# Performance work log

Hardware: AMD Instinct MI355X
Metric: run time of the kernel (lower is better)

The kernel has to match this reference:

```python
import jax, jax.numpy as jnp
import numpy as np

P = 16          # patch size (square)
HEADS = 8
DH = 64         # dim per head
SCALE = DH ** -0.5
EPS = 1e-5


def layernorm(x, g, b):
    mu = x.mean(-1, keepdims=True)
    var = ((x - mu) ** 2).mean(-1, keepdims=True)
    return (x - mu) * jax.lax.rsqrt(var + EPS) * g + b


def sattn(q, k, v):
    # q:[..., i, d], k/v:[..., j, d]; q already scaled
    sim = jnp.einsum('...id,...jd->...ij', q, k)
    a = jax.nn.softmax(sim, axis=-1)
    return jnp.einsum('...ij,...jd->...id', a, v)


def split_heads(t, b, N):
    return t.reshape(b, N, HEADS, DH).transpose(0, 2, 1, 3).reshape(b * HEADS, N, DH)


def merge_heads(t, b, N):
    return t.reshape(b, HEADS, N, DH).transpose(0, 2, 1, 3).reshape(b, N, HEADS * DH)


def qkv_cls(x, ln_g, ln_b, qkv_w):
    b, N, _ = x.shape
    xn = layernorm(x, ln_g, ln_b)
    q, k, v = jnp.split(xn @ qkv_w, 3, axis=-1)
    q = split_heads(q, b, N) * SCALE
    k = split_heads(k, b, N)
    v = split_heads(v, b, N)
    cls_out = sattn(q[:, :1], k, v)          # cls attends to everything
    return q[:, 1:], k[:, 1:], v[:, 1:], k[:, :1], v[:, :1], cls_out


def time_attention(x, ln_g, ln_b, qkv_w, out_w, out_b, f, n):
    b, N, _ = x.shape
    q_, k_, v_, cls_k, cls_v, cls_out = qkv_cls(x, ln_g, ln_b, qkv_w)
    bh = b * HEADS
    resh = lambda t: t.reshape(bh, f, n, DH).transpose(0, 2, 1, 3)  # 'b (f n) d -> (b n) f d' kept as [bh,n,f,d]
    q_, k_, v_ = resh(q_), resh(k_), resh(v_)
    ck = jnp.broadcast_to(cls_k[:, None], (bh, n, 1, DH))
    cv = jnp.broadcast_to(cls_v[:, None], (bh, n, 1, DH))
    out = sattn(q_, jnp.concatenate([ck, k_], 2), jnp.concatenate([cv, v_], 2))
    out = out.transpose(0, 2, 1, 3).reshape(bh, f * n, DH)
    out = jnp.concatenate([cls_out, out], axis=1)
    return merge_heads(out, b, N) @ out_w + out_b


def space_attention(x, ln_g, ln_b, qkv_w, out_w, out_b, f, n):
    b, N, _ = x.shape
    q_, k_, v_, cls_k, cls_v, cls_out = qkv_cls(x, ln_g, ln_b, qkv_w)
    bh = b * HEADS
    resh = lambda t: t.reshape(bh, f, n, DH)  # 'b (f n) d -> (b f) n d' kept as [bh,f,n,d]
    q_, k_, v_ = resh(q_), resh(k_), resh(v_)
    m = n // 2
    ck = jnp.broadcast_to(cls_k[:, None], (bh, f, 1, DH))
    cv = jnp.broadcast_to(cls_v[:, None], (bh, f, 1, DH))
    # mutual attention: first half queries attend to [cls, second half], and vice versa
    out1 = sattn(q_[:, :, :m], jnp.concatenate([ck, k_[:, :, m:]], 2), jnp.concatenate([cv, v_[:, :, m:]], 2))
    out2 = sattn(q_[:, :, m:], jnp.concatenate([ck, k_[:, :, :m]], 2), jnp.concatenate([cv, v_[:, :, :m]], 2))
    out = jnp.concatenate([out1, out2], axis=2).reshape(bh, f * n, DH)
    out = jnp.concatenate([cls_out, out], axis=1)
    return merge_heads(out, b, N) @ out_w + out_b


def geglu_ff(x, ln_g, ln_b, w1, b1, w2, b2):
    xn = layernorm(x, ln_g, ln_b)
    h = xn @ w1 + b1
    u, g = jnp.split(h, 2, axis=-1)
    return (u * jax.nn.gelu(g, approximate=False)) @ w2 + b2


def setup_inputs() -> dict:
    key = jax.random.key(0)
    ks = jax.random.split(key, 12)
    D, DEPTH, NC = 512, 12, 60
    inner = HEADS * DH
    B, F, C, H, W = 1, 4, 3, 480, 640
    n = (H // P) * (W // P)        # 1200
    N = F * n + 1                  # 4801
    pd = C * P * P                 # 768
    s = 0.02
    rn = lambda k, sh: jax.random.normal(k, sh, jnp.float32) * s
    z = lambda sh: jnp.zeros(sh, jnp.float32)
    o = lambda sh: jnp.ones(sh, jnp.float32)
    return {
        'video': jax.random.normal(ks[0], (B, F, C, H, W), jnp.float32),
        'patch_w': rn(ks[1], (pd, D)), 'patch_b': z((D,)),
        'pos_emb': rn(ks[2], (N, D)),
        'cls_token': rn(ks[3], (1, D)),
        't_ln_g': o((DEPTH, D)), 't_ln_b': z((DEPTH, D)),
        't_qkv_w': rn(ks[4], (DEPTH, D, 3 * inner)),
        't_out_w': rn(ks[5], (DEPTH, inner, D)), 't_out_b': z((DEPTH, D)),
        's_ln_g': o((DEPTH, D)), 's_ln_b': z((DEPTH, D)),
        's_qkv_w': rn(ks[6], (DEPTH, D, 3 * inner)),
        's_out_w': rn(ks[7], (DEPTH, inner, D)), 's_out_b': z((DEPTH, D)),
        'f_ln_g': o((DEPTH, D)), 'f_ln_b': z((DEPTH, D)),
        'f_w1': rn(ks[8], (DEPTH, D, 8 * D)), 'f_b1': z((DEPTH, 8 * D)),
        'f_w2': rn(ks[9], (DEPTH, 4 * D, D)), 'f_b2': z((DEPTH, D)),
        'o_ln_g': o((D,)), 'o_ln_b': z((D,)),
        'o_w': rn(ks[10], (D, NC)), 'o_b': z((NC,)),
    }


def reference(video, patch_w, patch_b, pos_emb, cls_token,
              t_ln_g, t_ln_b, t_qkv_w, t_out_w, t_out_b,
              s_ln_g, s_ln_b, s_qkv_w, s_out_w, s_out_b,
              f_ln_g, f_ln_b, f_w1, f_b1, f_w2, f_b2,
              o_ln_g, o_ln_b, o_w, o_b):
    b, f, c, H, W = video.shape
    hh, ww = H // P, W // P
    n = hh * ww
    wh = ww // 2
    half = W // 2

    def patchify(v):  # v: [b,f,c,H,W/2] -> [b, f*hh*wh, P*P*c]
        v = v.reshape(b, f, c, hh, P, wh, P)
        v = v.transpose(0, 1, 3, 5, 4, 6, 2)  # b f h w p1 p2 c
        return v.reshape(b, f * hh * wh, P * P * c)

    tok = jnp.concatenate([patchify(video[..., :half]), patchify(video[..., half:])], axis=1)
    tok = tok @ patch_w + patch_b
    x = jnp.concatenate([jnp.broadcast_to(cls_token[None], (b, 1, tok.shape[-1])), tok], axis=1)
    x = x + pos_emb[: x.shape[1]]

    depth = t_qkv_w.shape[0]
    for i in range(depth):
        x = time_attention(x, t_ln_g[i], t_ln_b[i], t_qkv_w[i], t_out_w[i], t_out_b[i], f, n) + x
        x = space_attention(x, s_ln_g[i], s_ln_b[i], s_qkv_w[i], s_out_w[i], s_out_b[i], f, n) + x
        x = geglu_ff(x, f_ln_g[i], f_ln_b[i], f_w1[i], f_b1[i], f_w2[i], f_b2[i]) + x

    cls = layernorm(x[:, 0], o_ln_g, o_ln_b)
    return cls @ o_w + o_b
```

## Files before the change

### kernel.cpp

```cpp
#include <hip/hip_runtime.h>
#include <cmath>


#define NT      4801
#define NP      4800
#define MP      4864
#define DM      512
#define QKV_ST  1536
#define LN_EPS  1e-5f
#define NCH     49

typedef __attribute__((ext_vector_type(8))) short bf16x8;
typedef __attribute__((ext_vector_type(4))) float f32x4;

__device__ __forceinline__ unsigned short f2b(float f) {
    union { float f; unsigned int u; } x; x.f = f;
    unsigned int r = (x.u + 0x7FFFu + ((x.u >> 16) & 1u)) >> 16;
    return (unsigned short)r;
}
__device__ __forceinline__ float b2f(unsigned short b) {
    union { unsigned int u; float f; } x; x.u = ((unsigned int)b) << 16;
    return x.f;
}
__device__ __forceinline__ unsigned int pack2(float a, float b) {
    return (unsigned int)f2b(a) | ((unsigned int)f2b(b) << 16);
}

__device__ __forceinline__ void gl_lds16(const void* g, void* l) {
    __builtin_amdgcn_global_load_lds(
        (__attribute__((address_space(1))) unsigned int*)(unsigned long long)(uintptr_t)g,
        (__attribute__((address_space(3))) unsigned int*)l, 16, 0, 0);
}

__device__ __forceinline__ void xcd_remap(int& bx, int& by, int& bz) {
    const int gx = gridDim.x, gy = gridDim.y;
    const int nwg = gx * gy * gridDim.z;
    const int orig = (blockIdx.z * gy + blockIdx.y) * gx + blockIdx.x;
    const int q = nwg >> 3, r = nwg & 7;
    const int xcd = orig & 7, idx = orig >> 3;
    const int id = (xcd < r ? xcd * (q + 1) : r * (q + 1) + (xcd - r) * q) + idx;
    bx = id % gx;
    const int t = id / gx;
    by = t % gy;
    bz = t / gy;
}

__global__ void patchify_kernel(const float* __restrict__ video, unsigned short* __restrict__ out)
{
    int idx = blockIdx.x * 256 + threadIdx.x;
    if (idx >= NP * 768) return;
    int tok = idx / 768, e = idx % 768;
    int c  = e % 3;
    int pe = e / 3;
    int p2 = pe % 16, p1 = pe / 16;
    int half = tok / 2400, r = tok % 2400;
    int f = r / 600, rr = r % 600;
    int hi = rr / 20, wi = rr % 20;
    int row = hi * 16 + p1;
    int col = half * 320 + wi * 16 + p2;
    out[idx] = f2b(video[(((size_t)f * 3 + c) * 480 + row) * 640 + col]);
}

__global__ void cls_init_kernel(const float* __restrict__ cls_token,
                                const float* __restrict__ pos, float* __restrict__ X)
{
    int d = blockIdx.x * 256 + threadIdx.x;
    if (d < DM) X[d] = cls_token[d] + pos[d];
}

__global__ void posx_init(const float* __restrict__ pos, float* __restrict__ X)
{
    int i = blockIdx.x * 256 + threadIdx.x;
    if (i < NP * DM / 4)
        ((float4*)(X + DM))[i] = ((const float4*)(pos + DM))[i];
}

__device__ __forceinline__ void transpose_tile(const float* __restrict__ in,
                                               unsigned short* __restrict__ out,
                                               int K, int N, int tile)
{
    __shared__ float T[32][33];
    int ntk = K / 32;
    int kt = tile % ntk, nt = tile / ntk;
    int k0 = kt * 32, n0 = nt * 32;
    int tx = threadIdx.x & 31, ty = threadIdx.x >> 5;
    #pragma unroll
    for (int i = 0; i < 4; i++)
        T[ty + 8 * i][tx] = in[(size_t)(k0 + ty + 8 * i) * N + n0 + tx];
    __syncthreads();
    #pragma unroll
    for (int i = 0; i < 4; i++)
        out[(size_t)(n0 + ty + 8 * i) * K + k0 + tx] = f2b(T[tx][ty + 8 * i]);
}

__global__ __launch_bounds__(256) void convertT_layer(
    const float* __restrict__ w0, const float* __restrict__ w1,
    const float* __restrict__ w2, const float* __restrict__ w3,
    const float* __restrict__ w4, const float* __restrict__ w5,
    unsigned short* __restrict__ out)
{
    int t = blockIdx.x;
    if      (t <  768) transpose_tile(w0, out + 0,       512, 1536, t);
    else if (t < 1024) transpose_tile(w1, out + 786432,  512,  512, t - 768);
    else if (t < 1792) transpose_tile(w2, out + 1048576, 512, 1536, t - 1024);
    else if (t < 2048) transpose_tile(w3, out + 1835008, 512,  512, t - 1792);
    else if (t < 4096) transpose_tile(w4, out + 2097152, 512, 4096, t - 2048);
    else               transpose_tile(w5, out + 4194304, 2048, 512, t - 4096);
}

__global__ __launch_bounds__(256) void convertT_one(
    const float* __restrict__ in, unsigned short* __restrict__ out, int K, int N)
{
    transpose_tile(in, out, K, N, blockIdx.x);
}

template<bool OB16>
__global__ __launch_bounds__(256, 2) void mfma_gemm(
    const unsigned short* __restrict__ A, const unsigned short* __restrict__ BT,
    const float* __restrict__ bias, const float* __restrict__ add,
    void* __restrict__ C, int Mv, int N, int K)
{
    __shared__ short Asm[2][128 * 64];
    __shared__ short Bsm[2][128 * 64];
    int bx, by, bz; xcd_remap(bx, by, bz); (void)bz;
    const int tid = threadIdx.x, w = tid >> 6, lane = tid & 63;
    const int row0 = by * 128, col0 = bx * 128;
    const int wm = w >> 1, wn = w & 1;
    const int l15 = lane & 15, quad = lane >> 4;

    f32x4 acc[4][4] = {};

    int ar[4], aq[4];
    #pragma unroll
    for (int i = 0; i < 4; i++) {
        int c = (w * 4 + i) * 64 + lane;
        ar[i] = c >> 3;
        aq[i] = (c & 7) ^ ((c >> 3) & 7);
    }
    const unsigned short* Ab = A  + (size_t)row0 * K;
    const unsigned short* Bb = BT + (size_t)col0 * K;

    #pragma unroll
    for (int i = 0; i < 4; i++) {
        gl_lds16(Ab + (size_t)ar[i] * K + aq[i] * 8, &Asm[0][(w * 4 + i) * 512]);
        gl_lds16(Bb + (size_t)ar[i] * K + aq[i] * 8, &Bsm[0][(w * 4 + i) * 512]);
    }

    const int nt = K >> 6;
    int cur = 0;
    for (int t = 0; t < nt; t++) {
        if (t + 1 < nt) {
            const int k0 = (t + 1) << 6;
            #pragma unroll
            for (int i = 0; i < 4; i++) {
                gl_lds16(Ab + (size_t)ar[i] * K + k0 + aq[i] * 8,
                         &Asm[cur ^ 1][(w * 4 + i) * 512]);
                gl_lds16(Bb + (size_t)ar[i] * K + k0 + aq[i] * 8,
                         &Bsm[cur ^ 1][(w * 4 + i) * 512]);
            }
            asm volatile("s_waitcnt vmcnt(8)\ns_barrier" ::: "memory");
        } else {
            asm volatile("s_waitcnt vmcnt(0)\ns_barrier" ::: "memory");
        }
        const short* As = Asm[cur];
        const short* Bs = Bsm[cur];
        #pragma unroll
        for (int ks = 0; ks < 2; ks++) {
            bf16x8 af[4], bfr[4];
            #pragma unroll
            for (int i = 0; i < 4; i++) {
                int m  = wm * 64 + i * 16 + l15;
                af[i]  = *(const bf16x8*)&As[m * 64 + (((ks * 4 + quad) ^ (m & 7))) * 8];
                int n  = wn * 64 + i * 16 + l15;
                bfr[i] = *(const bf16x8*)&Bs[n * 64 + (((ks * 4 + quad) ^ (n & 7))) * 8];
            }
            #pragma unroll
            for (int i = 0; i < 4; i++)
                #pragma unroll
                for (int j = 0; j < 4; j++)
                    acc[i][j] = __builtin_amdgcn_mfma_f32_16x16x32_bf16(
                                    af[i], bfr[j], acc[i][j], 0, 0, 0);
        }
        asm volatile("s_barrier" ::: "memory");
        cur ^= 1;
    }

    #pragma unroll
    for (int i = 0; i < 4; i++) {
        #pragma unroll
        for (int r = 0; r < 4; r++) {
            int row = row0 + wm * 64 + i * 16 + quad * 4 + r;
            if (row >= Mv) continue;
            #pragma unroll
            for (int j = 0; j < 4; j++) {
                int col = col0 + wn * 64 + j * 16 + l15;
                float v = acc[i][j][r];
                if (bias) v += bias[col];
                if (add)  v += add[(size_t)row * N + col];
                if (OB16) ((unsigned short*)C)[(size_t)row * N + col] = f2b(v);
                else      ((float*)C)[(size_t)row * N + col] = v;
            }
        }
    }
}

template<int SPLITS>
__global__ __launch_bounds__(256, 2) void mfma_gemm_sk(
    const unsigned short* __restrict__ A, const unsigned short* __restrict__ BT,
    const float* __restrict__ bias, float* __restrict__ C, int Mv, int N, int K)
{
    __shared__ short Asm[2][128 * 64];
    __shared__ short Bsm[2][128 * 64];
    int bx, by, bz; xcd_remap(bx, by, bz);
    const int tid = threadIdx.x, w = tid >> 6, lane = tid & 63;
    const int row0 = by * 128, col0 = bx * 128;
    const int wm = w >> 1, wn = w & 1;
    const int l15 = lane & 15, quad = lane >> 4;
    const int kchunk = K / SPLITS;
    const int kbeg = bz * kchunk;

    f32x4 acc[4][4] = {};

    int ar[4], aq[4];
    #pragma unroll
    for (int i = 0; i < 4; i++) {
        int c = (w * 4 + i) * 64 + lane;
        ar[i] = c >> 3;
        aq[i] = (c & 7) ^ ((c >> 3) & 7);
    }
    const unsigned short* Ab = A  + (size_t)row0 * K + kbeg;
    const unsigned short* Bb = BT + (size_t)col0 * K + kbeg;

    #pragma unroll
    for (int i = 0; i < 4; i++) {
        gl_lds16(Ab + (size_t)ar[i] * K + aq[i] * 8, &Asm[0][(w * 4 + i) * 512]);
        gl_lds16(Bb + (size_t)ar[i] * K + aq[i] * 8, &Bsm[0][(w * 4 + i) * 512]);
    }

    const int nt = kchunk >> 6;
    int cur = 0;
    for (int t = 0; t < nt; t++) {
        if (t + 1 < nt) {
            const int k0 = (t + 1) << 6;
            #pragma unroll
            for (int i = 0; i < 4; i++) {
                gl_lds16(Ab + (size_t)ar[i] * K + k0 + aq[i] * 8,
                         &Asm[cur ^ 1][(w * 4 + i) * 512]);
                gl_lds16(Bb + (size_t)ar[i] * K + k0 + aq[i] * 8,
                         &Bsm[cur ^ 1][(w * 4 + i) * 512]);
            }
            asm volatile("s_waitcnt vmcnt(8)\ns_barrier" ::: "memory");
        } else {
            asm volatile("s_waitcnt vmcnt(0)\ns_barrier" ::: "memory");
        }
        const short* As = Asm[cur];
        const short* Bs = Bsm[cur];
        #pragma unroll
        for (int ks = 0; ks < 2; ks++) {
            bf16x8 af[4], bfr[4];
            #pragma unroll
            for (int i = 0; i < 4; i++) {
                int m  = wm * 64 + i * 16 + l15;
                af[i]  = *(const bf16x8*)&As[m * 64 + (((ks * 4 + quad) ^ (m & 7))) * 8];
                int n  = wn * 64 + i * 16 + l15;
                bfr[i] = *(const bf16x8*)&Bs[n * 64 + (((ks * 4 + quad) ^ (n & 7))) * 8];
            }
            #pragma unroll
            for (int i = 0; i < 4; i++)
                #pragma unroll
                for (int j = 0; j < 4; j++)
                    acc[i][j] = __builtin_amdgcn_mfma_f32_16x16x32_bf16(
                                    af[i], bfr[j], acc[i][j], 0, 0, 0);
        }
        asm volatile("s_barrier" ::: "memory");
        cur ^= 1;
    }

    const bool addb = (bz == 0) && (bias != nullptr);
    #pragma unroll
    for (int i = 0; i < 4; i++) {
        #pragma unroll
        for (int r = 0; r < 4; r++) {
            int row = row0 + wm * 64 + i * 16 + quad * 4 + r;
            if (row >= Mv) continue;
            #pragma unroll
            for (int j = 0; j < 4; j++) {
                int col = col0 + wn * 64 + j * 16 + l15;
                float v = acc[i][j][r];
                if (addb) v += bias[col];
                unsafeAtomicAdd(&C[(size_t)row * N + col], v);
            }
        }
    }
}

__global__ __launch_bounds__(256, 2) void mfma_ff1_geglu(
    const unsigned short* __restrict__ A, const unsigned short* __restrict__ BT,
    const float* __restrict__ b1, unsigned short* __restrict__ out, int Mv)
{
    __shared__ short Asm[128 * 64];
    __shared__ short Bu[128 * 64];
    __shared__ short Bg[128 * 64];
    int bx, by, bz; xcd_remap(bx, by, bz); (void)bz;
    const int tid = threadIdx.x, w = tid >> 6, lane = tid & 63;
    const int row0 = by * 128, colu0 = bx * 128;
    const int wm = w >> 1, wn = w & 1;
    const int l15 = lane & 15, quad = lane >> 4;

    f32x4 au[4][4] = {};
    f32x4 ag[4][4] = {};

    int ar[4], aq[4];
    #pragma unroll
    for (int i = 0; i < 4; i++) {
        int c = (w * 4 + i) * 64 + lane;
        ar[i] = c >> 3;
        aq[i] = (c & 7) ^ ((c >> 3) & 7);
    }
    const unsigned short* Ab  = A  + (size_t)row0 * 512;
    const unsigned short* Bub = BT + (size_t)colu0 * 512;
    const unsigned short* Bgb = BT + (size_t)(colu0 + 2048) * 512;

    for (int k0 = 0; k0 < 512; k0 += 64) {
        #pragma unroll
        for (int i = 0; i < 4; i++) {
            gl_lds16(Ab  + (size_t)ar[i] * 512 + k0 + aq[i] * 8, &Asm[(w * 4 + i) * 512]);
            gl_lds16(Bub + (size_t)ar[i] * 512 + k0 + aq[i] * 8, &Bu[(w * 4 + i) * 512]);
            gl_lds16(Bgb + (size_t)ar[i] * 512 + k0 + aq[i] * 8, &Bg[(w * 4 + i) * 512]);
        }
        __syncthreads();
        #pragma unroll
        for (int ks = 0; ks < 2; ks++) {
            bf16x8 af[4], bu[4], bg[4];
            #pragma unroll
            for (int i = 0; i < 4; i++) {
                int m = wm * 64 + i * 16 + l15;
                int p = (((ks * 4 + quad) ^ (m & 7))) * 8;
                af[i] = *(const bf16x8*)&Asm[m * 64 + p];
                int n = wn * 64 + i * 16 + l15;
                int pb = (((ks * 4 + quad) ^ (n & 7))) * 8;
                bu[i] = *(const bf16x8*)&Bu[n * 64 + pb];
                bg[i] = *(const bf16x8*)&Bg[n * 64 + pb];
            }
            #pragma unroll
            for (int i = 0; i < 4; i++)
                #pragma unroll
                for (int j = 0; j < 4; j++) {
                    au[i][j] = __builtin_amdgcn_mfma_f32_16x16x32_bf16(
                                   af[i], bu[j], au[i][j], 0, 0, 0);
                    ag[i][j] = __builtin_amdgcn_mfma_f32_16x16x32_bf16(
                                   af[i], bg[j], ag[i][j], 0, 0, 0);
                }
        }
        __syncthreads();
    }

    #pragma unroll
    for (int i = 0; i < 4; i++) {
        #pragma unroll
        for (int r = 0; r < 4; r++) {
            int row = row0 + wm * 64 + i * 16 + quad * 4 + r;
            if (row >= Mv) continue;
            #pragma unroll
            for (int j = 0; j < 4; j++) {
                int col = colu0 + wn * 64 + j * 16 + l15;
                float u = au[i][j][r] + b1[col];
                float g = ag[i][j][r] + b1[col + 2048];
                float h = u * 0.5f * g * (1.f + erff(g * 0.70710678f));
                out[(size_t)row * 2048 + col] = f2b(h);
            }
        }
    }
}

__global__ __launch_bounds__(256) void ln_bf16(
    const float* __restrict__ x, const float* __restrict__ g,
    const float* __restrict__ b, unsigned short* __restrict__ y, int M)
{
    int wid = threadIdx.x >> 6, lane = threadIdx.x & 63;
    int row = blockIdx.x * 4 + wid;
    if (row >= M) return;
    const float4* xr = (const float4*)(x + (size_t)row * DM);
    float4 v0 = xr[lane * 2], v1 = xr[lane * 2 + 1];
    float s  = v0.x + v0.y + v0.z + v0.w + v1.x + v1.y + v1.z + v1.w;
    float s2 = v0.x*v0.x + v0.y*v0.y + v0.z*v0.z + v0.w*v0.w
             + v1.x*v1.x + v1.y*v1.y + v1.z*v1.z + v1.w*v1.w;
    #pragma unroll
    for (int off = 32; off >= 1; off >>= 1) {
        s  += __shfl_xor(s, off);
        s2 += __shfl_xor(s2, off);
    }
    float mu = s * (1.f / DM);
    float var = s2 * (1.f / DM) - mu * mu;
    float r = rsqrtf(var + LN_EPS);
    const float4* gv = (const float4*)g;
    const float4* bv = (const float4*)b;
    unsigned int* yr = (unsigned int*)(y + (size_t)row * DM);
    #pragma unroll
    for (int i = 0; i < 2; i++) {
        float4 v = (i == 0) ? v0 : v1;
        float4 gg = gv[lane * 2 + i], bb = bv[lane * 2 + i];
        float ox = (v.x - mu) * r * gg.x + bb.x;
        float oy = (v.y - mu) * r * gg.y + bb.y;
        float oz = (v.z - mu) * r * gg.z + bb.z;
        float ow = (v.w - mu) * r * gg.w + bb.w;
        yr[lane * 4 + i * 2 + 0] = pack2(ox, oy);
        yr[lane * 4 + i * 2 + 1] = pack2(oz, ow);
    }
}

__global__ __launch_bounds__(256, 4) void time_attn4(
    const unsigned short* __restrict__ qkv, unsigned short* __restrict__ out)
{
    int tid = threadIdx.x;
    int dq = tid & 3, tl = tid >> 2;
    int b = blockIdx.x;
    int h = b / 75;
    int j = (b - h * 75) * 64 + tl;
    int pos = j % 1200;
    int d0 = dq * 16;
    union { bf16x8 v; unsigned short u[8]; } ld;
    float q[16];
    const unsigned short* qp = qkv + (size_t)(j + 1) * QKV_ST + h * 64 + d0;
    #pragma unroll
    for (int c = 0; c < 2; c++) {
        ld.v = *(const bf16x8*)(qp + c * 8);
        #pragma unroll
        for (int e = 0; e < 8; e++) q[c * 8 + e] = b2f(ld.u[e]) * 0.125f;
    }
    int rows[5] = {0, pos + 1, pos + 1201, pos + 2401, pos + 3601};
    float s[5];
    #pragma unroll
    for (int kk = 0; kk < 5; kk++) {
        const unsigned short* kp = qkv + (size_t)rows[kk] * QKV_ST + 512 + h * 64 + d0;
        float ss = 0.f;
        #pragma unroll
        for (int c = 0; c < 2; c++) {
            ld.v = *(const bf16x8*)(kp + c * 8);
            #pragma unroll
            for (int e = 0; e < 8; e++) ss += q[c * 8 + e] * b2f(ld.u[e]);
        }
        ss += __shfl_xor(ss, 1);
        ss += __shfl_xor(ss, 2);
        s[kk] = ss;
    }
    float mx = s[0];
    #pragma unroll
    for (int kk = 1; kk < 5; kk++) mx = fmaxf(mx, s[kk]);
    float e5[5], l = 0.f;
    #pragma unroll
    for (int kk = 0; kk < 5; kk++) { e5[kk] = __expf(s[kk] - mx); l += e5[kk]; }
    float rl = 1.f / l;
    float acc[16];
    #pragma unroll
    for (int d = 0; d < 16; d++) acc[d] = 0.f;
    #pragma unroll
    for (int kk = 0; kk < 5; kk++) {
        float p = e5[kk] * rl;
        const unsigned short* vp = qkv + (size_t)rows[kk] * QKV_ST + 1024 + h * 64 + d0;
        #pragma unroll
        for (int c = 0; c < 2; c++) {
            ld.v = *(const bf16x8*)(vp + c * 8);
            #pragma unroll
            for (int e = 0; e < 8; e++) acc[c * 8 + e] += p * b2f(ld.u[e]);
        }
    }
    unsigned int* op = (unsigned int*)(out + (size_t)(j + 1) * DM + h * 64 + d0);
    #pragma unroll
    for (int d2 = 0; d2 < 8; d2++) op[d2] = pack2(acc[2 * d2], acc[2 * d2 + 1]);
}

#define SPAD 72
__global__ __launch_bounds__(256, 2) void space_attn_mfma(
    const unsigned short* __restrict__ qkv, unsigned short* __restrict__ out)
{
    __shared__ short Ksm[64 * SPAD];
    __shared__ short VTsm[64 * SPAD];
    __shared__ short Psm[4][32 * SPAD];
    int qt = blockIdx.x, h = blockIdx.y, g = blockIdx.z;
    int f = g >> 1, half = g & 1;
    int tid = threadIdx.x, w = tid >> 6, lane = tid & 63;
    int l15 = lane & 15, quad = lane >> 4;

    int qrow_base = qt * 128 + w * 32;
    int qb = 1 + f * 1200 + half * 600;
    int kb = 1 + f * 1200 + (1 - half) * 600;

    bf16x8 aQ[2][2];
    #pragma unroll
    for (int mf = 0; mf < 2; mf++) {
        int qr = qrow_base + mf * 16 + l15;
        int qtok = qb + ((qr < 600) ? qr : 0);
        const unsigned short* qp = qkv + (size_t)qtok * QKV_ST + h * 64;
        #pragma unroll
        for (int ks = 0; ks < 2; ks++)
            aQ[mf][ks] = *(const bf16x8*)(qp + ks * 32 + quad * 8);
    }

    f32x4 O[2][4] = {};
    float mrow[2][4], lrow[2][4];
    #pragma unroll
    for (int mf = 0; mf < 2; mf++)
        #pragma unroll
        for (int r = 0; r < 4; r++) { mrow[mf][r] = -1e30f; lrow[mf][r] = 0.f; }

    for (int kt = 0; kt < 10; kt++) {
        __syncthreads();
        #pragma unroll
        for (int it = 0; it < 2; it++) {
            int c = tid + it * 256;
            int row = c >> 3, dc = (c & 7) * 8;
            int kidx = kt * 64 + row;
            int tok = (kidx == 0) ? 0 : ((kidx <= 600) ? kb + kidx - 1 : 0);
            const unsigned short* kp = qkv + (size_t)tok * QKV_ST + 512 + h * 64 + dc;
            *(bf16x8*)&Ksm[row * SPAD + dc] = *(const bf16x8*)kp;
            union { bf16x8 v; unsigned short u[8]; } vv;
            vv.v = *(const bf16x8*)(kp + 512);
            #pragma unroll
            for (int e = 0; e < 8; e++)
                VTsm[(dc + e) * SPAD + row] = vv.u[e];
        }
        __syncthreads();

        f32x4 S[2][4] = {};
        #pragma unroll
        for (int ks = 0; ks < 2; ks++) {
            bf16x8 bK[4];
            #pragma unroll
            for (int nf = 0; nf < 4; nf++)
                bK[nf] = *(const bf16x8*)&Ksm[(nf * 16 + l15) * SPAD + ks * 32 + quad * 8];
            #pragma unroll
            for (int mf = 0; mf < 2; mf++)
                #pragma unroll
                for (int nf = 0; nf < 4; nf++)
                    S[mf][nf] = __builtin_amdgcn_mfma_f32_16x16x32_bf16(
                                    aQ[mf][ks], bK[nf], S[mf][nf], 0, 0, 0);
        }

        #pragma unroll
        for (int mf = 0; mf < 2; mf++) {
            float pv[4][4];
            float lm[4] = {-1e30f, -1e30f, -1e30f, -1e30f};
            #pragma unroll
            for (int nf = 0; nf < 4; nf++) {
                int kidx = kt * 64 + nf * 16 + l15;
                bool valid = kidx <= 600;
                #pragma unroll
                for (int r = 0; r < 4; r++) {
                    float s = valid ? S[mf][nf][r] * 0.125f : -1e30f;
                    pv[nf][r] = s;
                    lm[r] = fmaxf(lm[r], s);
                }
            }
            #pragma unroll
            for (int off = 1; off < 16; off <<= 1)
                #pragma unroll
                for (int r = 0; r < 4; r++)
                    lm[r] = fmaxf(lm[r], __shfl_xor(lm[r], off));
            #pragma unroll
            for (int r = 0; r < 4; r++) {
                float nm = fmaxf(mrow[mf][r], lm[r]);
                float c = __expf(mrow[mf][r] - nm);
                mrow[mf][r] = nm;
                lrow[mf][r] *= c;
                #pragma unroll
                for (int nf = 0; nf < 4; nf++) O[mf][nf][r] *= c;
            }
            float rs[4] = {0.f, 0.f, 0.f, 0.f};
            #pragma unroll
            for (int nf = 0; nf < 4; nf++)
                #pragma unroll
                for (int r = 0; r < 4; r++) {
                    float p = __expf(pv[nf][r] - mrow[mf][r]);
                    pv[nf][r] = p;
                    rs[r] += p;
                }
            #pragma unroll
            for (int off = 1; off < 16; off <<= 1)
                #pragma unroll
                for (int r = 0; r < 4; r++)
                    rs[r] += __shfl_xor(rs[r], off);
            #pragma unroll
            for (int r = 0; r < 4; r++) lrow[mf][r] += rs[r];
            #pragma unroll
            for (int nf = 0; nf < 4; nf++)
                #pragma unroll
                for (int r = 0; r < 4; r++)
                    Psm[w][(mf * 16 + quad * 4 + r) * SPAD + nf * 16 + l15] = (short)f2b(pv[nf][r]);
        }
        asm volatile("s_waitcnt lgkmcnt(0)" ::: "memory");

        #pragma unroll
        for (int ks2 = 0; ks2 < 2; ks2++) {
            bf16x8 aP[2], bV[4];
            #pragma unroll
            for (int mf = 0; mf < 2; mf++)
                aP[mf] = *(const bf16x8*)&Psm[w][(mf * 16 + l15) * SPAD + ks2 * 32 + quad * 8];
            #pragma unroll
            for (int nf = 0; nf < 4; nf++)
                bV[nf] = *(const bf16x8*)&VTsm[(nf * 16 + l15) * SPAD + ks2 * 32 + quad * 8];
            #pragma unroll
            for (int mf = 0; mf < 2; mf++)
                #pragma unroll
                for (int nf = 0; nf < 4; nf++)
                    O[mf][nf] = __builtin_amdgcn_mfma_f32_16x16x32_bf16(
                                    aP[mf], bV[nf], O[mf][nf], 0, 0, 0);
        }
    }

    #pragma unroll
    for (int mf = 0; mf < 2; mf++)
        #pragma unroll
        for (int r = 0; r < 4; r++) {
            int qr = qrow_base + mf * 16 + quad * 4 + r;
            if (qr >= 600) continue;
            int qtok = qb + qr;
            float rl = 1.f / lrow[mf][r];
            #pragma unroll
            for (int nf = 0; nf < 4; nf++)
                out[(size_t)qtok * DM + h * 64 + nf * 16 + l15] = f2b(O[mf][nf][r] * rl);
        }
}

__global__ __launch_bounds__(256) void cls_attn_part(
    const unsigned short* __restrict__ qkv, float* __restrict__ part)
{
    int ch = blockIdx.x, h = blockIdx.y;
    int wid = threadIdx.x >> 6, lane = threadIdx.x & 63;
    __shared__ float sm[4], sl[4], sa[4][64];
    float qv = b2f(qkv[h * 64 + lane]) * 0.125f;
    int k0 = ch * 100 + wid * 25;
    float m = -1e30f, l = 0.f, acc = 0.f;
    for (int i = 0; i < 25; i += 2) {
        int key0 = k0 + i, key1 = key0 + 1;
        bool ok0 = key0 < NT;
        bool ok1 = (i + 1 < 25) && (key1 < NT);
        const unsigned short* kr0 = qkv + (size_t)(ok0 ? key0 : 0) * QKV_ST + 512 + h * 64;
        const unsigned short* kr1 = qkv + (size_t)(ok1 ? key1 : 0) * QKV_ST + 512 + h * 64;
        float s0 = qv * b2f(kr0[lane]);
        float v0 = b2f(kr0[512 + lane]);
        float s1 = qv * b2f(kr1[lane]);
        float v1 = b2f(kr1[512 + lane]);
        #pragma unroll
        for (int off = 32; off >= 1; off >>= 1) {
            s0 += __shfl_xor(s0, off);
            s1 += __shfl_xor(s1, off);
        }
        float nm = m;
        if (ok0) nm = fmaxf(nm, s0);
        if (ok1) nm = fmaxf(nm, s1);
        float c  = __expf(m - nm);
        float p0 = ok0 ? __expf(s0 - nm) : 0.f;
        float p1 = ok1 ? __expf(s1 - nm) : 0.f;
        l   = l * c + p0 + p1;
        acc = acc * c + p0 * v0 + p1 * v1;
        m = nm;
    }
    if (lane == 0) { sm[wid] = m; sl[wid] = l; }
    sa[wid][lane] = acc;
    __syncthreads();
    if (wid == 0) {
        float M2 = fmaxf(fmaxf(sm[0], sm[1]), fmaxf(sm[2], sm[3]));
        float L = 0.f, o = 0.f;
        #pragma unroll
        for (int w = 0; w < 4; w++) {
            float c = __expf(sm[w] - M2);
            L += sl[w] * c;
            o += sa[w][lane] * c;
        }
        float* p = part + ((size_t)h * NCH + ch) * 68;
        if (lane == 0) { p[0] = M2; p[1] = L; }
        p[4 + lane] = o;
    }
}

__global__ __launch_bounds__(64) void cls_attn_reduce(
    const float* __restrict__ part, unsigned short* __restrict__ out)
{
    int h = blockIdx.x, lane = threadIdx.x;
    float m = -1e30f, l = 0.f, acc = 0.f;
    for (int c = 0; c < NCH; c++) {
        const float* p = part + ((size_t)h * NCH + c) * 68;
        float cm = p[0], cl = p[1], ca = p[4 + lane];
        float nm = fmaxf(m, cm);
        float e1 = __expf(m - nm), e2 = __expf(cm - nm);
        l   = l * e1 + cl * e2;
        acc = acc * e1 + ca * e2;
        m = nm;
    }
    out[h * 64 + lane] = f2b(acc / l);
}

__global__ __launch_bounds__(64) void head_kernel(
    const float* __restrict__ x, const float* __restrict__ g,
    const float* __restrict__ b, const float* __restrict__ w,
    const float* __restrict__ ob, float* __restrict__ out)
{
    __shared__ float xn[DM];
    int lane = threadIdx.x;
    const float4* xr = (const float4*)x;
    float4 v0 = xr[lane * 2], v1 = xr[lane * 2 + 1];
    float s  = v0.x + v0.y + v0.z + v0.w + v1.x + v1.y + v1.z + v1.w;
    float s2 = v0.x*v0.x + v0.y*v0.y + v0.z*v0.z + v0.w*v0.w
             + v1.x*v1.x + v1.y*v1.y + v1.z*v1.z + v1.w*v1.w;
    #pragma unroll
    for (int off = 32; off >= 1; off >>= 1) {
        s  += __shfl_xor(s, off);
        s2 += __shfl_xor(s2, off);
    }
    float mu = s * (1.f / DM);
    float var = s2 * (1.f / DM) - mu * mu;
    float r = rsqrtf(var + LN_EPS);
    #pragma unroll
    for (int i = 0; i < 8; i++) {
        int d = lane * 8 + i;
        xn[d] = (x[d] - mu) * r * g[d] + b[d];
    }
    __syncthreads();
    if (lane < 60) {
        float a = ob[lane];
        for (int d = 0; d < DM; d++) a += xn[d] * w[d * 60 + lane];
        out[lane] = a;
    }
}

extern "C" void kernel_launch(void* const* d_in, const int* in_sizes, int n_in,
                              void* d_out, int out_size, void* d_ws, size_t ws_size,
                              hipStream_t stream)
{
    const float* video     = (const float*)d_in[0];
    const float* patch_w   = (const float*)d_in[1];
    const float* patch_b   = (const float*)d_in[2];
    const float* pos_emb   = (const float*)d_in[3];
    const float* cls_token = (const float*)d_in[4];
    const float* t_ln_g    = (const float*)d_in[5];
    const float* t_ln_b    = (const float*)d_in[6];
    const float* t_qkv_w   = (const float*)d_in[7];
    const float* t_out_w   = (const float*)d_in[8];
    const float* t_out_b   = (const float*)d_in[9];
    const float* s_ln_g    = (const float*)d_in[10];
    const float* s_ln_b    = (const float*)d_in[11];
    const float* s_qkv_w   = (const float*)d_in[12];
    const float* s_out_w   = (const float*)d_in[13];
    const float* s_out_b   = (const float*)d_in[14];
    const float* f_ln_g    = (const float*)d_in[15];
    const float* f_ln_b    = (const float*)d_in[16];
    const float* f_w1      = (const float*)d_in[17];
    const float* f_b1      = (const float*)d_in[18];
    const float* f_w2      = (const float*)d_in[19];
    const float* f_b2      = (const float*)d_in[20];
    const float* o_ln_g    = (const float*)d_in[21];
    const float* o_ln_b    = (const float*)d_in[22];
    const float* o_w       = (const float*)d_in[23];
    const float* o_b       = (const float*)d_in[24];

    char* ws = (char*)d_ws;
    size_t o = 0;
    float*          X    = (float*)(ws + o);          o += (size_t)(MP + 1) * 512 * 4;
    unsigned short* XN   = (unsigned short*)(ws + o); o += (size_t)MP * 512 * 2;
    unsigned short* QKV  = (unsigned short*)(ws + o); o += (size_t)MP * 1536 * 2;
    unsigned short* H16  = (unsigned short*)(ws + o); o += (size_t)MP * 4096 * 2;
    unsigned short* MID  = (unsigned short*)(ws + o); o += (size_t)MP * 2048 * 2;
    unsigned short* PT   = (unsigned short*)(ws + o); o += (size_t)MP * 768 * 2;
    unsigned short* W16  = (unsigned short*)(ws + o); o += (size_t)5242880 * 2;
    unsigned short* PW16 = (unsigned short*)(ws + o); o += (size_t)512 * 768 * 2;
    float*          CP   = (float*)(ws + o);          o += (size_t)8 * NCH * 68 * 4;

    patchify_kernel<<<(NP * 768 + 255) / 256, 256, 0, stream>>>(video, PT);
    cls_init_kernel<<<2, 256, 0, stream>>>(cls_token, pos_emb, X);
    posx_init<<<NP * DM / 4 / 256, 256, 0, stream>>>(pos_emb, X);
    convertT_one<<<(768 / 32) * (512 / 32), 256, 0, stream>>>(patch_w, PW16, 768, 512);
    mfma_gemm_sk<3><<<dim3(4, 38, 3), 256, 0, stream>>>(PT, PW16, patch_b,
                                                        X + DM, NP, DM, 768);

    dim3 g_qkv(12, 38), g_ff1(16, 38);
    dim3 g_out_sk(4, 38, 2), g_ff2_sk(4, 38, 4);
    for (int i = 0; i < 12; i++) {
        convertT_layer<<<5120, 256, 0, stream>>>(
            t_qkv_w + (size_t)i * 512 * 1536, t_out_w + (size_t)i * 512 * 512,
            s_qkv_w + (size_t)i * 512 * 1536, s_out_w + (size_t)i * 512 * 512,
            f_w1 + (size_t)i * 512 * 4096, f_w2 + (size_t)i * 2048 * 512, W16);

        ln_bf16<<<1201, 256, 0, stream>>>(X, t_ln_g + i * DM, t_ln_b + i * DM, XN, NT);
        mfma_gemm<true><<<g_qkv, 256, 0, stream>>>(XN, W16 + 0, nullptr, nullptr,
                                                   QKV, NT, QKV_ST, DM);
        time_attn4<<<600, 256, 0, stream>>>(QKV, MID);
        cls_attn_part<<<dim3(NCH, 8), 256, 0, stream>>>(QKV, CP);
        cls_attn_reduce<<<8, 64, 0, stream>>>(CP, MID);
        mfma_gemm_sk<2><<<g_out_sk, 256, 0, stream>>>(MID, W16 + 786432, t_out_b + i * DM,
                                                      X, NT, DM, DM);
        ln_bf16<<<1201, 256, 0, stream>>>(X, s_ln_g + i * DM, s_ln_b + i * DM, XN, NT);
        mfma_gemm<true><<<g_qkv, 256, 0, stream>>>(XN, W16 + 1048576, nullptr, nullptr,
                                                   QKV, NT, QKV_ST, DM);
        space_attn_mfma<<<dim3(5, 8, 8), 256, 0, stream>>>(QKV, MID);
        cls_attn_part<<<dim3(NCH, 8), 256, 0, stream>>>(QKV, CP);
        cls_attn_reduce<<<8, 64, 0, stream>>>(CP, MID);
        mfma_gemm_sk<2><<<g_out_sk, 256, 0, stream>>>(MID, W16 + 1835008, s_out_b + i * DM,
                                                      X, NT, DM, DM);
        ln_bf16<<<1201, 256, 0, stream>>>(X, f_ln_g + i * DM, f_ln_b + i * DM, XN, NT);
        mfma_ff1_geglu<<<g_ff1, 256, 0, stream>>>(XN, W16 + 2097152, f_b1 + i * 4096,
                                                  MID, NT);
        mfma_gemm_sk<4><<<g_ff2_sk, 256, 0, stream>>>(MID, W16 + 4194304, f_b2 + i * DM,
                                                      X, NT, DM, 2048);
    }

    head_kernel<<<1, 64, 0, stream>>>(X, o_ln_g, o_ln_b, o_w, o_b, (float*)d_out);
}
```

Measured before the change: 4.383 ms.

## Double-buffer GEGLU FF1 GEMM loads and remap split-K blocks per XCD

```diff
diff --git a/kernel.cpp b/kernel.cpp
--- a/kernel.cpp
+++ b/kernel.cpp
@@ -43,6 +43,17 @@
     const int t = id / gx;
     by = t % gy;
     bz = t / gy;
+}
+
+__device__ __forceinline__ void xcd_remap_sk(int& bx, int& by, int& bz) {
+    const int gx = gridDim.x, gy = gridDim.y;
+    const int tpx = (gx * gy) >> 3;
+    const int L = (blockIdx.z * gy + blockIdx.y) * gx + blockIdx.x;
+    const int c = L & 7, k = L >> 3;
+    bz = k / tpx;
+    const int t = c * tpx + (k - bz * tpx);
+    bx = t % gx;
+    by = t / gx;
 }
 
 __global__ void patchify_kernel(const float* __restrict__ video, unsigned short* __restrict__ out)
@@ -211,7 +222,7 @@
 {
     __shared__ short Asm[2][128 * 64];
     __shared__ short Bsm[2][128 * 64];
-    int bx, by, bz; xcd_remap(bx, by, bz);
+    int bx, by, bz; xcd_remap_sk(bx, by, bz);
     const int tid = threadIdx.x, w = tid >> 6, lane = tid & 63;
     const int row0 = by * 128, col0 = bx * 128;
     const int wm = w >> 1, wn = w & 1;
@@ -294,13 +305,13 @@
     }
 }
 
-__global__ __launch_bounds__(256, 2) void mfma_ff1_geglu(
+__global__ __launch_bounds__(256, 1) void mfma_ff1_geglu(
     const unsigned short* __restrict__ A, const unsigned short* __restrict__ BT,
     const float* __restrict__ b1, unsigned short* __restrict__ out, int Mv)
 {
-    __shared__ short Asm[128 * 64];
-    __shared__ short Bu[128 * 64];
-    __shared__ short Bg[128 * 64];
+    __shared__ short Asm[2][128 * 64];
+    __shared__ short Bu[2][128 * 64];
+    __shared__ short Bg[2][128 * 64];
     int bx, by, bz; xcd_remap(bx, by, bz); (void)bz;
     const int tid = threadIdx.x, w = tid >> 6, lane = tid & 63;
     const int row0 = by * 128, colu0 = bx * 128;
@@ -321,14 +332,33 @@
     const unsigned short* Bub = BT + (size_t)colu0 * 512;
     const unsigned short* Bgb = BT + (size_t)(colu0 + 2048) * 512;
 
-    for (int k0 = 0; k0 < 512; k0 += 64) {
-        #pragma unroll
-        for (int i = 0; i < 4; i++) {
-            gl_lds16(Ab  + (size_t)ar[i] * 512 + k0 + aq[i] * 8, &Asm[(w * 4 + i) * 512]);
-            gl_lds16(Bub + (size_t)ar[i] * 512 + k0 + aq[i] * 8, &Bu[(w * 4 + i) * 512]);
-            gl_lds16(Bgb + (size_t)ar[i] * 512 + k0 + aq[i] * 8, &Bg[(w * 4 + i) * 512]);
-        }
-        __syncthreads();
+    #pragma unroll
+    for (int i = 0; i < 4; i++) {
+        gl_lds16(Ab  + (size_t)ar[i] * 512 + aq[i] * 8, &Asm[0][(w * 4 + i) * 512]);
+        gl_lds16(Bub + (size_t)ar[i] * 512 + aq[i] * 8, &Bu[0][(w * 4 + i) * 512]);
+        gl_lds16(Bgb + (size_t)ar[i] * 512 + aq[i] * 8, &Bg[0][(w * 4 + i) * 512]);
+    }
+
+    int cur = 0;
+    for (int t = 0; t < 8; t++) {
+        if (t + 1 < 8) {
+            const int k0 = (t + 1) << 6;
+            #pragma unroll
+            for (int i = 0; i < 4; i++) {
+                gl_lds16(Ab  + (size_t)ar[i] * 512 + k0 + aq[i] * 8,
+                         &Asm[cur ^ 1][(w * 4 + i) * 512]);
+                gl_lds16(Bub + (size_t)ar[i] * 512 + k0 + aq[i] * 8,
+                         &Bu[cur ^ 1][(w * 4 + i) * 512]);
+                gl_lds16(Bgb + (size_t)ar[i] * 512 + k0 + aq[i] * 8,
+                         &Bg[cur ^ 1][(w * 4 + i) * 512]);
+            }
+            asm volatile("s_waitcnt vmcnt(12)\ns_barrier" ::: "memory");
+        } else {
+            asm volatile("s_waitcnt vmcnt(0)\ns_barrier" ::: "memory");
+        }
+        const short* As = Asm[cur];
+        const short* Bus = Bu[cur];
+        const short* Bgs = Bg[cur];
         #pragma unroll
         for (int ks = 0; ks < 2; ks++) {
             bf16x8 af[4], bu[4], bg[4];
@@ -336,11 +366,11 @@
             for (int i = 0; i < 4; i++) {
                 int m = wm * 64 + i * 16 + l15;
                 int p = (((ks * 4 + quad) ^ (m & 7))) * 8;
-                af[i] = *(const bf16x8*)&Asm[m * 64 + p];
+                af[i] = *(const bf16x8*)&As[m * 64 + p];
                 int n = wn * 64 + i * 16 + l15;
                 int pb = (((ks * 4 + quad) ^ (n & 7))) * 8;
-                bu[i] = *(const bf16x8*)&Bu[n * 64 + pb];
-                bg[i] = *(const bf16x8*)&Bg[n * 64 + pb];
+                bu[i] = *(const bf16x8*)&Bus[n * 64 + pb];
+                bg[i] = *(const bf16x8*)&Bgs[n * 64 + pb];
             }
             #pragma unroll
             for (int i = 0; i < 4; i++)
@@ -352,7 +382,8 @@
                                    af[i], bg[j], ag[i][j], 0, 0, 0);
                 }
         }
-        __syncthreads();
+        asm volatile("s_barrier" ::: "memory");
+        cur ^= 1;
     }
 
     #pragma unroll
```

New measurement: 4.378 ms. No clear change (-0.1%).
